# Optimization experiments

Measured on AMD Instinct MI355X. Metric: run time of the kernel, lower is better.

## Reference

```python
import jax, jax.numpy as jnp
import numpy as np

STATE_DIM = 128
ACT_DIM = 32
ENC_K = 10   # encoder_spine_dim
DEC_K = 10   # decoder_dim
H0, H1 = 2048, 2048
BATCH = 16384
MAX_ACTION = 1.0
STD0 = 0.3872983346207417  # sqrt(0.15)


def setup_inputs() -> dict:
    key = jax.random.key(0)
    ks = jax.random.split(key, 10)
    state = jax.random.normal(ks[0], (BATCH, STATE_DIM), dtype=jnp.float32)
    # encoder params: mean linspace over mean_range, std constant
    mean_enc = jnp.broadcast_to(jnp.linspace(-3.0, 3.0, ENC_K, dtype=jnp.float32),
                                (1, STATE_DIM, ENC_K))
    std_enc = jnp.full((1, STATE_DIM, ENC_K), STD0, dtype=jnp.float32)
    def lin(k, fan_in, fan_out):
        bound = 1.0 / np.sqrt(fan_in)
        k1, k2 = jax.random.split(k)
        W = jax.random.uniform(k1, (fan_out, fan_in), jnp.float32, -bound, bound)
        b = jax.random.uniform(k2, (fan_out,), jnp.float32, -bound, bound)
        return W, b
    W1, b1 = lin(ks[1], STATE_DIM * ENC_K, H0)
    W2, b2 = lin(ks[2], H0, H1)
    W3, b3 = lin(ks[3], H1, ACT_DIM * DEC_K)
    # grouped conv1d: weight [act_dim, 1, dec_k], bias [act_dim]
    bound = 1.0 / np.sqrt(DEC_K)
    Wd = jax.random.uniform(ks[4], (ACT_DIM, 1, DEC_K), jnp.float32, -bound, bound)
    bd = jax.random.uniform(ks[5], (ACT_DIM,), jnp.float32, -bound, bound)
    return {"state": state, "mean_enc": mean_enc, "std_enc": std_enc,
            "W1": W1, "b1": b1, "W2": W2, "b2": b2, "W3": W3, "b3": b3,
            "Wd": Wd, "bd": bd}


def reference(state, mean_enc, std_enc, W1, b1, W2, b2, W3, b3, Wd, bd):
    # Population-coding encoder: sigmoid((obs - mean)/std), flattened
    spine = jax.nn.sigmoid((state[:, :, None] - mean_enc) / std_enc)  # [B, D, K]
    spine = spine.reshape(state.shape[0], -1)                         # [B, D*K]
    a = jax.nn.relu(spine @ W1.T + b1)
    a = jax.nn.relu(a @ W2.T + b2)
    a = a @ W3.T + b3                                                 # [B, A*Kd]
    d = a.reshape(-1, ACT_DIM, DEC_K)                                 # [B, A, Kd]
    # grouped Conv1d with kernel == length => per-channel dot product
    raw = jnp.einsum('bak,ak->ba', d, Wd[:, 0, :]) + bd               # [B, A]
    return MAX_ACTION * jnp.tanh(raw)
```

## Files before the change

kernel.cpp:

```cpp
#include <hip/hip_runtime.h>
#include <hip/hip_bf16.h>
#include <stdint.h>

#define BATCH   16384
#define SDIM    128
#define ENCK    10
#define ADIM    32
#define DECK    10
#define HID     2048
#define KSPINE  1280

typedef __bf16 bf16x8 __attribute__((ext_vector_type(8)));
typedef float  f32x4  __attribute__((ext_vector_type(4)));

typedef __attribute__((address_space(1))) const void kGlobalVoid;
typedef __attribute__((address_space(3))) void       kLdsVoid;

__device__ __forceinline__ unsigned short f2b(float f) {
  union { float f; unsigned u; } v; v.f = f;
  unsigned r = v.u + 0x7fffu + ((v.u >> 16) & 1u);
  return (unsigned short)(r >> 16);
}

__global__ void f2b_kernel(const float* __restrict__ in, unsigned* __restrict__ out, int n2) {
  int i = blockIdx.x * blockDim.x + threadIdx.x;
  if (i >= n2) return;
  float2 v = reinterpret_cast<const float2*>(in)[i];
  out[i] = (unsigned)f2b(v.x) | ((unsigned)f2b(v.y) << 16);
}

__global__ void encoder_kernel(const float* __restrict__ state,
                               const float* __restrict__ mean,
                               const float* __restrict__ stdv,
                               unsigned* __restrict__ spine) {
  int idx = blockIdx.x * blockDim.x + threadIdx.x;
  if (idx >= BATCH * SDIM) return;
  int d = idx & (SDIM - 1);
  float x = state[idx];
  float vals[ENCK];
#pragma unroll
  for (int k = 0; k < ENCK; ++k) {
    float z = (x - mean[d * ENCK + k]) / stdv[d * ENCK + k];
    vals[k] = 1.f / (1.f + __expf(-z));
  }
  unsigned* dst = spine + idx * (ENCK / 2);
#pragma unroll
  for (int k = 0; k < ENCK / 2; ++k)
    dst[k] = (unsigned)f2b(vals[2 * k]) | ((unsigned)f2b(vals[2 * k + 1]) << 16);
}

__global__ void weff_kernel(const float* __restrict__ W3, const float* __restrict__ Wd,
                            unsigned short* __restrict__ Weff) {
  int idx = blockIdx.x * 256 + threadIdx.x;
  int a = idx >> 11, j = idx & 2047;
  float s = 0.f;
#pragma unroll
  for (int k = 0; k < DECK; ++k)
    s += Wd[a * DECK + k] * W3[(size_t)(a * DECK + k) * HID + j];
  Weff[idx] = f2b(s);
}

__global__ void beff_kernel(const float* __restrict__ b3, const float* __restrict__ Wd,
                            const float* __restrict__ bd, float* __restrict__ beff) {
  int a = threadIdx.x;
  if (a >= ADIM) return;
  float s = bd[a];
#pragma unroll
  for (int k = 0; k < DECK; ++k) s += Wd[a * DECK + k] * b3[a * DECK + k];
  beff[a] = s;
}


#define A0B 0
#define B0B 32768
#define A1B 65536
#define B1B 98304

#define FENCE asm volatile("" ::: "memory")

#define STAGE(BASEPTR, R0A, R0B, LDS0, LDS1, KT)                                             \
  __builtin_amdgcn_global_load_lds((kGlobalVoid*)((BASEPTR) + (size_t)((R0A) + rs) * K + (KT) + ce), \
                                   (kLdsVoid*)(smem + (LDS0) + t * 16), 16, 0, 0);           \
  __builtin_amdgcn_global_load_lds((kGlobalVoid*)((BASEPTR) + (size_t)((R0B) + rs) * K + (KT) + ce), \
                                   (kLdsVoid*)(smem + (LDS1) + t * 16), 16, 0, 0);

#define DS_AF(DST, ABASE, MPN)                                                               \
  _Pragma("unroll")                                                                          \
  for (int j2 = 0; j2 < 2; ++j2) {                                                           \
    _Pragma("unroll")                                                                        \
    for (int ks = 0; ks < 2; ++ks) {                                                         \
      int rowl = wr * 128 + (MPN) * 32 + j2 * 16 + lr;                                       \
      DST[j2][ks] = *reinterpret_cast<const bf16x8*>(                                        \
          smem + (ABASE) + rowl * 128 + ((((ks) << 6) | (kh << 4)) ^ swz));                  \
    }                                                                                        \
  }

#define DS_BF(DST, BBASE)                                                                    \
  _Pragma("unroll")                                                                          \
  for (int n = 0; n < 4; ++n) {                                                              \
    _Pragma("unroll")                                                                        \
    for (int ks = 0; ks < 2; ++ks) {                                                         \
      int rowl = wc * 64 + n * 16 + lr;                                                      \
      DST[n][ks] = *reinterpret_cast<const bf16x8*>(                                         \
          smem + (BBASE) + rowl * 128 + ((((ks) << 6) | (kh << 4)) ^ swz));                  \
    }                                                                                        \
  }

#define MFMA16(MP, AF, BF)                                                                   \
  _Pragma("unroll")                                                                          \
  for (int j2 = 0; j2 < 2; ++j2)                                                             \
    _Pragma("unroll")                                                                        \
    for (int n = 0; n < 4; ++n)                                                              \
      _Pragma("unroll")                                                                      \
      for (int ks = 0; ks < 2; ++ks)                                                         \
        acc[(MP) * 2 + j2][n] = __builtin_amdgcn_mfma_f32_16x16x32_bf16(                     \
            AF[j2][ks], BF[n][ks], acc[(MP) * 2 + j2][n], 0, 0, 0);

#define PH(MP, AF_CUR, AF_NXT, BF_CUR, NXT_ABASE, NXT_MP, DOVM, DOB, NXT_BF, NXT_BBASE, STG) \
  do {                                                                                       \
    asm volatile("s_waitcnt lgkmcnt(0)" ::: "memory");                                       \
    __builtin_amdgcn_sched_barrier(0);                                                       \
    if (DOVM) {                                                                              \
      asm volatile("s_waitcnt vmcnt(6)" ::: "memory");                                       \
      __builtin_amdgcn_sched_barrier(0);                                                     \
    }                                                                                        \
    __builtin_amdgcn_s_setprio(1);                                                           \
    MFMA16(MP, AF_CUR, BF_CUR);                                                              \
    __builtin_amdgcn_s_setprio(0);                                                           \
    DS_AF(AF_NXT, NXT_ABASE, NXT_MP);                                                        \
    if (DOB) { DS_BF(NXT_BF, NXT_BBASE); }                                                   \
    STG;                                                                                     \
    FENCE;                                                                                   \
    __builtin_amdgcn_s_barrier();                                                            \
  } while (0)

__global__ __launch_bounds__(512, 2) void gemm256(
    const unsigned short* __restrict__ A,
    const unsigned short* __restrict__ Bw,
    const float* __restrict__ bias,
    unsigned short* __restrict__ Cout,
    int K, int NI) {
  __shared__ char smem[131072];

  const int t    = threadIdx.x;
  const int lane = t & 63;
  const int w    = t >> 6;
  const int wr   = w >> 2;
  const int wc   = w & 3;
  const int lr   = lane & 15;
  const int kh   = lane >> 4;
  const int swz  = (lr & 7) << 4;
  const int rs   = t >> 3;
  const int ce   = ((t & 7) ^ (rs & 7)) << 3;

  const int bid = blockIdx.x;
  const int xcd = bid & 7, idx = bid >> 3;
  const int row0 = (xcd * 8 + (idx >> 3)) * 256;
  const int col0 = (idx & 7) * 256;

  f32x4 acc[8][4];
#pragma unroll
  for (int m = 0; m < 8; ++m)
#pragma unroll
    for (int n = 0; n < 4; ++n)
      acc[m][n] = (f32x4){0.f, 0.f, 0.f, 0.f};

  bf16x8 af0[2][2], af1[2][2], bfv0[4][2], bfv1[4][2];

  STAGE(Bw, col0 + 0,   col0 + 64,  B0B + 0,     B0B + 8192,  0);
  STAGE(Bw, col0 + 128, col0 + 192, B0B + 16384, B0B + 24576, 0);
  STAGE(A,  row0 + 0,   row0 + 128, A0B + 0,     A0B + 16384, 0);
  STAGE(A,  row0 + 64,  row0 + 192, A0B + 8192,  A0B + 24576, 0);
  STAGE(Bw, col0 + 0,   col0 + 64,  B1B + 0,     B1B + 8192,  64);
  STAGE(Bw, col0 + 128, col0 + 192, B1B + 16384, B1B + 24576, 64);
  STAGE(A,  row0 + 0,   row0 + 128, A1B + 0,     A1B + 16384, 64);
  asm volatile("s_waitcnt vmcnt(6)" ::: "memory");
  FENCE;
  __builtin_amdgcn_s_barrier();
  DS_AF(af0, A0B, 0);
  DS_BF(bfv0, B0B);

  for (int i = 0; i < NI; ++i) {
    int kt0 = i << 7;
    int kt1 = kt0 + 64;
    int kt2 = kt0 + 128; if (kt2 >= K) kt2 -= K;
    int kt3 = kt0 + 192; if (kt3 >= K) kt3 -= K;

    PH(0, af0, af1, bfv0, A0B, 1, false, false, bfv1, B1B,
       STAGE(A,  row0 + 64,  row0 + 192, A1B + 8192,  A1B + 24576, kt1));
    PH(1, af1, af0, bfv0, A0B, 2, false, false, bfv1, B1B,
       STAGE(Bw, col0 + 0,   col0 + 64,  B0B + 0,     B0B + 8192,  kt2));
    PH(2, af0, af1, bfv0, A0B, 3, false, false, bfv1, B1B,
       STAGE(Bw, col0 + 128, col0 + 192, B0B + 16384, B0B + 24576, kt2));
    PH(3, af1, af0, bfv0, A1B, 0, true,  true,  bfv1, B1B,
       STAGE(A,  row0 + 0,   row0 + 128, A0B + 0,     A0B + 16384, kt2));
    PH(0, af0, af1, bfv1, A1B, 1, false, false, bfv0, B0B,
       STAGE(A,  row0 + 64,  row0 + 192, A0B + 8192,  A0B + 24576, kt2));
    PH(1, af1, af0, bfv1, A1B, 2, false, false, bfv0, B0B,
       STAGE(Bw, col0 + 0,   col0 + 64,  B1B + 0,     B1B + 8192,  kt3));
    PH(2, af0, af1, bfv1, A1B, 3, false, false, bfv0, B0B,
       STAGE(Bw, col0 + 128, col0 + 192, B1B + 16384, B1B + 24576, kt3));
    PH(3, af1, af0, bfv1, A0B, 0, true,  true,  bfv0, B0B,
       STAGE(A,  row0 + 0,   row0 + 128, A1B + 0,     A1B + 16384, kt3));
  }

#pragma unroll
  for (int m = 0; m < 8; ++m) {
    int gr0 = row0 + wr * 128 + m * 16 + kh * 4;
#pragma unroll
    for (int n = 0; n < 4; ++n) {
      int gc = col0 + wc * 64 + n * 16 + lr;
      float bv = bias[gc];
#pragma unroll
      for (int v = 0; v < 4; ++v) {
        float val = fmaxf(acc[m][n][v] + bv, 0.f);
        Cout[(size_t)(gr0 + v) * 2048 + gc] = f2b(val);
      }
    }
  }
}

__global__ __launch_bounds__(128) void gemm_skinny(
    const unsigned short* __restrict__ A,
    const unsigned short* __restrict__ Bw,
    const float* __restrict__ beff,
    float* __restrict__ out) {
  const int t = threadIdx.x, lane = t & 63, w = t >> 6;
  const int lr = lane & 15, kh = lane >> 4;
  const int row0 = (blockIdx.x * 2 + w) * 16;
  f32x4 acc[2];
  acc[0] = (f32x4){0.f, 0.f, 0.f, 0.f};
  acc[1] = (f32x4){0.f, 0.f, 0.f, 0.f};

  const unsigned short* Arow = A  + (size_t)(row0 + lr) * HID + kh * 8;
  const unsigned short* B0   = Bw + (size_t)(lr) * HID + kh * 8;
  const unsigned short* B1   = Bw + (size_t)(16 + lr) * HID + kh * 8;

#pragma unroll 4
  for (int kt = 0; kt < HID; kt += 32) {
    bf16x8 a  = *reinterpret_cast<const bf16x8*>(Arow + kt);
    bf16x8 b0 = *reinterpret_cast<const bf16x8*>(B0 + kt);
    bf16x8 b1 = *reinterpret_cast<const bf16x8*>(B1 + kt);
    acc[0] = __builtin_amdgcn_mfma_f32_16x16x32_bf16(a, b0, acc[0], 0, 0, 0);
    acc[1] = __builtin_amdgcn_mfma_f32_16x16x32_bf16(a, b1, acc[1], 0, 0, 0);
  }
#pragma unroll
  for (int n = 0; n < 2; ++n)
#pragma unroll
    for (int v = 0; v < 4; ++v) {
      int row = row0 + kh * 4 + v;
      int col = n * 16 + lr;
      out[(size_t)row * ADIM + col] = tanhf(acc[n][v] + beff[col]);
    }
}

extern "C" void kernel_launch(void* const* d_in, const int* in_sizes, int n_in,
                              void* d_out, int out_size, void* d_ws, size_t ws_size,
                              hipStream_t stream) {
  const float* state    = (const float*)d_in[0];
  const float* mean_enc = (const float*)d_in[1];
  const float* std_enc  = (const float*)d_in[2];
  const float* W1 = (const float*)d_in[3];
  const float* b1 = (const float*)d_in[4];
  const float* W2 = (const float*)d_in[5];
  const float* b2 = (const float*)d_in[6];
  const float* W3 = (const float*)d_in[7];
  const float* b3 = (const float*)d_in[8];
  const float* Wd = (const float*)d_in[9];
  const float* bd = (const float*)d_in[10];

  char* ws = (char*)d_ws;
  unsigned short* W1b   = (unsigned short*)(ws + 0);
  unsigned short* W2b   = (unsigned short*)(ws + 5242880);
  unsigned short* Weff  = (unsigned short*)(ws + 13631488);
  float*          beff  = (float*)(ws + 13762560);
  unsigned short* spine = (unsigned short*)(ws + 13762688);
  unsigned short* h1    = (unsigned short*)(ws + 55705728);
  unsigned short* h2    = (unsigned short*)(ws + 122814592);

  f2b_kernel<<<5120, 256, 0, stream>>>(W1, (unsigned*)W1b, 1310720);
  f2b_kernel<<<8192, 256, 0, stream>>>(W2, (unsigned*)W2b, 2097152);
  weff_kernel<<<256, 256, 0, stream>>>(W3, Wd, Weff);
  beff_kernel<<<1, 64, 0, stream>>>(b3, Wd, bd, beff);

  encoder_kernel<<<(BATCH * SDIM) / 256, 256, 0, stream>>>(state, mean_enc, std_enc, (unsigned*)spine);

  gemm256<<<512, 512, 0, stream>>>(spine, W1b, b1, h1, KSPINE, KSPINE / 128);
  gemm256<<<512, 512, 0, stream>>>(h1,    W2b, b2, h2, HID,    HID / 128);
  gemm_skinny<<<BATCH / 32, 128, 0, stream>>>(h2, Weff, beff, (float*)d_out);
}
```

Measured before the change: 249.3 us.

## Restructure GEMM main loop into quadrant-based 8-phase schedule with fewer fragment registers

Replaces the 4-phase register double-buffered PH schedule with an 8-phase-per-tile schedule. Each phase loads a 64-row A quadrant and half of the B fragments, then issues a 16-MFMA quadrant block, with barriers separating LDS reads, global-to-LDS staging and compute. This reuses A/B fragments across adjacent quadrants so fewer fragment registers are live, and it changes the vmcnt wait depth and the prologue staging order. The cost is extra barriers per tile and LDS reads no longer prefetched under the previous MFMAs.

```diff
diff --git a/kernel.cpp b/kernel.cpp
--- a/kernel.cpp
+++ b/kernel.cpp
@@ -84,55 +84,43 @@
   __builtin_amdgcn_global_load_lds((kGlobalVoid*)((BASEPTR) + (size_t)((R0B) + rs) * K + (KT) + ce), \
                                    (kLdsVoid*)(smem + (LDS1) + t * 16), 16, 0, 0);
 
-#define DS_AF(DST, ABASE, MPN)                                                               \
+#define DS_A4(DST, ABASE, Q)                                                                 \
   _Pragma("unroll")                                                                          \
-  for (int j2 = 0; j2 < 2; ++j2) {                                                           \
+  for (int j = 0; j < 4; ++j) {                                                              \
     _Pragma("unroll")                                                                        \
     for (int ks = 0; ks < 2; ++ks) {                                                         \
-      int rowl = wr * 128 + (MPN) * 32 + j2 * 16 + lr;                                       \
-      DST[j2][ks] = *reinterpret_cast<const bf16x8*>(                                        \
+      int rowl = wr * 128 + (Q) * 64 + j * 16 + lr;                                          \
+      DST[j][ks] = *reinterpret_cast<const bf16x8*>(                                         \
           smem + (ABASE) + rowl * 128 + ((((ks) << 6) | (kh << 4)) ^ swz));                  \
     }                                                                                        \
   }
 
-#define DS_BF(DST, BBASE)                                                                    \
+#define DS_B2(DST, BBASE, NH)                                                                \
   _Pragma("unroll")                                                                          \
-  for (int n = 0; n < 4; ++n) {                                                              \
+  for (int n = 0; n < 2; ++n) {                                                              \
     _Pragma("unroll")                                                                        \
     for (int ks = 0; ks < 2; ++ks) {                                                         \
-      int rowl = wc * 64 + n * 16 + lr;                                                      \
+      int rowl = wc * 64 + ((NH) * 2 + n) * 16 + lr;                                         \
       DST[n][ks] = *reinterpret_cast<const bf16x8*>(                                         \
           smem + (BBASE) + rowl * 128 + ((((ks) << 6) | (kh << 4)) ^ swz));                  \
     }                                                                                        \
   }
 
-#define MFMA16(MP, AF, BF)                                                                   \
+#define MFMAQ(Q, NH, AF, BF)                                                                 \
   _Pragma("unroll")                                                                          \
-  for (int j2 = 0; j2 < 2; ++j2)                                                             \
+  for (int j = 0; j < 4; ++j)                                                                \
     _Pragma("unroll")                                                                        \
-    for (int n = 0; n < 4; ++n)                                                              \
+    for (int n = 0; n < 2; ++n)                                                              \
       _Pragma("unroll")                                                                      \
       for (int ks = 0; ks < 2; ++ks)                                                         \
-        acc[(MP) * 2 + j2][n] = __builtin_amdgcn_mfma_f32_16x16x32_bf16(                     \
-            AF[j2][ks], BF[n][ks], acc[(MP) * 2 + j2][n], 0, 0, 0);
-
-#define PH(MP, AF_CUR, AF_NXT, BF_CUR, NXT_ABASE, NXT_MP, DOVM, DOB, NXT_BF, NXT_BBASE, STG) \
-  do {                                                                                       \
-    asm volatile("s_waitcnt lgkmcnt(0)" ::: "memory");                                       \
-    __builtin_amdgcn_sched_barrier(0);                                                       \
-    if (DOVM) {                                                                              \
-      asm volatile("s_waitcnt vmcnt(6)" ::: "memory");                                       \
-      __builtin_amdgcn_sched_barrier(0);                                                     \
-    }                                                                                        \
-    __builtin_amdgcn_s_setprio(1);                                                           \
-    MFMA16(MP, AF_CUR, BF_CUR);                                                              \
-    __builtin_amdgcn_s_setprio(0);                                                           \
-    DS_AF(AF_NXT, NXT_ABASE, NXT_MP);                                                        \
-    if (DOB) { DS_BF(NXT_BF, NXT_BBASE); }                                                   \
-    STG;                                                                                     \
-    FENCE;                                                                                   \
-    __builtin_amdgcn_s_barrier();                                                            \
-  } while (0)
+        acc[(Q) * 4 + j][(NH) * 2 + n] = __builtin_amdgcn_mfma_f32_16x16x32_bf16(            \
+            AF[j][ks], BF[n][ks], acc[(Q) * 4 + j][(NH) * 2 + n], 0, 0, 0);
+
+#define BAR __builtin_amdgcn_s_barrier()
+#define LGKM0 do { asm volatile("s_waitcnt lgkmcnt(0)" ::: "memory"); \
+                   __builtin_amdgcn_sched_barrier(0); } while (0)
+#define VM4 do { asm volatile("s_waitcnt vmcnt(4)" ::: "memory"); \
+                 __builtin_amdgcn_sched_barrier(0); } while (0)
 
 __global__ __launch_bounds__(512, 2) void gemm256(
     const unsigned short* __restrict__ A,
@@ -165,20 +153,17 @@
     for (int n = 0; n < 4; ++n)
       acc[m][n] = (f32x4){0.f, 0.f, 0.f, 0.f};
 
-  bf16x8 af0[2][2], af1[2][2], bfv0[4][2], bfv1[4][2];
-
+  bf16x8 afq[4][2], bf01[2][2], bf23[2][2];
+
+  STAGE(A,  row0 + 0,   row0 + 64,  A0B + 0,     A0B + 8192,  0);
+  STAGE(A,  row0 + 128, row0 + 192, A0B + 16384, A0B + 24576, 0);
   STAGE(Bw, col0 + 0,   col0 + 64,  B0B + 0,     B0B + 8192,  0);
   STAGE(Bw, col0 + 128, col0 + 192, B0B + 16384, B0B + 24576, 0);
-  STAGE(A,  row0 + 0,   row0 + 128, A0B + 0,     A0B + 16384, 0);
-  STAGE(A,  row0 + 64,  row0 + 192, A0B + 8192,  A0B + 24576, 0);
   STAGE(Bw, col0 + 0,   col0 + 64,  B1B + 0,     B1B + 8192,  64);
   STAGE(Bw, col0 + 128, col0 + 192, B1B + 16384, B1B + 24576, 64);
-  STAGE(A,  row0 + 0,   row0 + 128, A1B + 0,     A1B + 16384, 64);
-  asm volatile("s_waitcnt vmcnt(6)" ::: "memory");
+  VM4;
   FENCE;
-  __builtin_amdgcn_s_barrier();
-  DS_AF(af0, A0B, 0);
-  DS_BF(bfv0, B0B);
+  BAR;
 
   for (int i = 0; i < NI; ++i) {
     int kt0 = i << 7;
@@ -186,23 +171,49 @@
     int kt2 = kt0 + 128; if (kt2 >= K) kt2 -= K;
     int kt3 = kt0 + 192; if (kt3 >= K) kt3 -= K;
 
-    PH(0, af0, af1, bfv0, A0B, 1, false, false, bfv1, B1B,
-       STAGE(A,  row0 + 64,  row0 + 192, A1B + 8192,  A1B + 24576, kt1));
-    PH(1, af1, af0, bfv0, A0B, 2, false, false, bfv1, B1B,
-       STAGE(Bw, col0 + 0,   col0 + 64,  B0B + 0,     B0B + 8192,  kt2));
-    PH(2, af0, af1, bfv0, A0B, 3, false, false, bfv1, B1B,
-       STAGE(Bw, col0 + 128, col0 + 192, B0B + 16384, B0B + 24576, kt2));
-    PH(3, af1, af0, bfv0, A1B, 0, true,  true,  bfv1, B1B,
-       STAGE(A,  row0 + 0,   row0 + 128, A0B + 0,     A0B + 16384, kt2));
-    PH(0, af0, af1, bfv1, A1B, 1, false, false, bfv0, B0B,
-       STAGE(A,  row0 + 64,  row0 + 192, A0B + 8192,  A0B + 24576, kt2));
-    PH(1, af1, af0, bfv1, A1B, 2, false, false, bfv0, B0B,
-       STAGE(Bw, col0 + 0,   col0 + 64,  B1B + 0,     B1B + 8192,  kt3));
-    PH(2, af0, af1, bfv1, A1B, 3, false, false, bfv0, B0B,
-       STAGE(Bw, col0 + 128, col0 + 192, B1B + 16384, B1B + 24576, kt3));
-    PH(3, af1, af0, bfv1, A0B, 0, true,  true,  bfv0, B0B,
-       STAGE(A,  row0 + 0,   row0 + 128, A1B + 0,     A1B + 16384, kt3));
-  }
+    DS_A4(afq, A0B, 0); DS_B2(bf01, B0B, 0);
+    STAGE(A,  row0 + 0,   row0 + 64,  A1B + 0,     A1B + 8192,  kt1);
+    FENCE; BAR; LGKM0;
+    __builtin_amdgcn_s_setprio(1); MFMAQ(0, 0, afq, bf01); __builtin_amdgcn_s_setprio(0);
+    FENCE; BAR;
+    DS_B2(bf23, B0B, 1);
+    STAGE(A,  row0 + 128, row0 + 192, A1B + 16384, A1B + 24576, kt1);
+    FENCE; BAR; LGKM0;
+    __builtin_amdgcn_s_setprio(1); MFMAQ(0, 1, afq, bf23); __builtin_amdgcn_s_setprio(0);
+    FENCE; BAR;
+    DS_A4(afq, A0B, 1);
+    STAGE(Bw, col0 + 0,   col0 + 64,  B0B + 0,     B0B + 8192,  kt2);
+    FENCE; BAR; LGKM0;
+    __builtin_amdgcn_s_setprio(1); MFMAQ(1, 1, afq, bf23); __builtin_amdgcn_s_setprio(0);
+    FENCE; BAR;
+    STAGE(Bw, col0 + 128, col0 + 192, B0B + 16384, B0B + 24576, kt2);
+    FENCE; BAR;
+    __builtin_amdgcn_s_setprio(1); MFMAQ(1, 0, afq, bf01); __builtin_amdgcn_s_setprio(0);
+    VM4;
+    FENCE; BAR;
+
+    DS_A4(afq, A1B, 0); DS_B2(bf01, B1B, 0);
+    STAGE(A,  row0 + 0,   row0 + 64,  A0B + 0,     A0B + 8192,  kt2);
+    FENCE; BAR; LGKM0;
+    __builtin_amdgcn_s_setprio(1); MFMAQ(0, 0, afq, bf01); __builtin_amdgcn_s_setprio(0);
+    FENCE; BAR;
+    DS_B2(bf23, B1B, 1);
+    STAGE(A,  row0 + 128, row0 + 192, A0B + 16384, A0B + 24576, kt2);
+    FENCE; BAR; LGKM0;
+    __builtin_amdgcn_s_setprio(1); MFMAQ(0, 1, afq, bf23); __builtin_amdgcn_s_setprio(0);
+    FENCE; BAR;
+    DS_A4(afq, A1B, 1);
+    STAGE(Bw, col0 + 0,   col0 + 64,  B1B + 0,     B1B + 8192,  kt3);
+    FENCE; BAR; LGKM0;
+    __builtin_amdgcn_s_setprio(1); MFMAQ(1, 1, afq, bf23); __builtin_amdgcn_s_setprio(0);
+    FENCE; BAR;
+    STAGE(Bw, col0 + 128, col0 + 192, B1B + 16384, B1B + 24576, kt3);
+    FENCE; BAR;
+    __builtin_amdgcn_s_setprio(1); MFMAQ(1, 0, afq, bf01); __builtin_amdgcn_s_setprio(0);
+    VM4;
+    FENCE; BAR;
+  }
+  asm volatile("s_waitcnt vmcnt(0)" ::: "memory");
 
 #pragma unroll
   for (int m = 0; m < 8; ++m) {
```

Measured after the change: 255.1 us. 1.02x slower.
